# Performance work log

Measured on AMD Instinct MI355X. Metric: run time of the kernel, lower is better.

## Reference

```python
import jax, jax.numpy as jnp
import numpy as np

N = 4096
DIM = 128      # dim_in
HID = 256      # mlp hidden_dim
K_IN = 8       # k for linear_k

def _knn_edges(dist, k):
    # dist: [n,n]; k nearest neighbors excluding self (matches heapq loop)
    n = dist.shape[0]
    d = jnp.where(jnp.eye(n, dtype=bool), jnp.inf, dist)
    nbr = jax.lax.top_k(-d, k)[1]                     # [n,k] indices of k smallest
    src = jnp.repeat(jnp.arange(n), k)                # res[0] = i
    dst = nbr.reshape(-1)                             # res[1] = neighbor
    return src, dst

def _gcn_conv(x, src, dst, W, b):
    # torch_geometric GCNConv: add self loops + symmetric normalization
    n = x.shape[0]
    loop = jnp.arange(n)
    s = jnp.concatenate([src, loop])
    t = jnp.concatenate([dst, loop])
    xw = x @ W
    deg = jax.ops.segment_sum(jnp.ones(s.shape[0], x.dtype), t, num_segments=n)
    dinv = jax.lax.rsqrt(deg)                         # deg >= 1 due to self loops
    norm = dinv[s] * dinv[t]
    out = jax.ops.segment_sum(norm[:, None] * xw[s], t, num_segments=n)
    return out + b

def _gcn(x, src, dst, Wg1, bg1, Wg2, bg2):
    h = jax.nn.relu(_gcn_conv(x, src, dst, Wg1, bg1))
    h = _gcn_conv(h, src, dst, Wg2, bg2)              # dropout is identity in eval
    return jax.nn.log_softmax(h, axis=1)

def _conv2d(x, w, b):
    y = jax.lax.conv_general_dilated(x, w, (1, 1), 'SAME',
        dimension_numbers=('NCHW', 'OIHW', 'NCHW'))
    return y + b.reshape(1, -1, 1, 1)

def setup_inputs():
    key = jax.random.key(0)
    ks = jax.random.split(key, 20)
    f32 = jnp.float32
    def w(k, shape):
        fan = shape[0]
        return (jax.random.uniform(k, shape, f32) * 2 - 1) * (1.0 / np.sqrt(fan))
    return {
        'data_x_1': jax.random.normal(ks[0], (1, N, 4), f32),
        'data_x_2': jax.random.normal(ks[1], (1, N, K_IN, 4), f32),
        'Wk': w(ks[2], (K_IN, 1)),        'bk': jnp.zeros((1,), f32),
        'Wg1': w(ks[3], (8, DIM // 2)),   'bg1': jnp.zeros((DIM // 2,), f32),
        'Wg2': w(ks[4], (DIM // 2, DIM)), 'bg2': jnp.zeros((DIM,), f32),
        'Wq': w(ks[5], (3 * DIM, DIM)),   'bq': jnp.zeros((DIM,), f32),
        'Wkey': w(ks[6], (3 * DIM, DIM)), 'bkey': jnp.zeros((DIM,), f32),
        'Woff': w(ks[7], (4, DIM)),       'boff': jnp.zeros((DIM,), f32),
        'pw': jnp.full((1,), 0.25, f32),
        'Wf1': w(ks[8], (DIM, HID)),      'bf1': jnp.zeros((HID,), f32),
        'Wf2': w(ks[9], (HID, HID)),      'bf2': jnp.zeros((HID,), f32),
        'Wf3': w(ks[10], (HID, 4)),       'bf3': jnp.zeros((4,), f32),
        'Wcy3': w(ks[11], (1, 1, 1, 3)),  'bcy3': jnp.zeros((1,), f32),
        'Wcx3': w(ks[12], (1, 1, 3, 1)),  'bcx3': jnp.zeros((1,), f32),
        'Wcy5': w(ks[13], (1, 1, 1, 5)),  'bcy5': jnp.zeros((1,), f32),
        'Wcx5': w(ks[14], (1, 1, 5, 1)),  'bcx5': jnp.zeros((1,), f32),
        'Wcy9': w(ks[15], (1, 1, 1, 9)),  'bcy9': jnp.zeros((1,), f32),
        'Wcx9': w(ks[16], (1, 1, 9, 1)),  'bcx9': jnp.zeros((1,), f32),
    }

def reference(data_x_1, data_x_2, Wk, bk, Wg1, bg1, Wg2, bg2, Wq, bq, Wkey, bkey,
              Woff, boff, pw, Wf1, bf1, Wf2, bf2, Wf3, bf3,
              Wcy3, bcy3, Wcx3, bcx3, Wcy5, bcy5, Wcx5, bcx5, Wcy9, bcy9, Wcx9, bcx9):
    # linear_k over k dimension: [1,n,k,4] -> transpose -> [1,n,4,k] -> [1,n,4]
    dx2 = jnp.swapaxes(data_x_2, 2, 3)
    dx2_out = (dx2 @ Wk + bk)[..., 0]
    data_x = jnp.concatenate([data_x_1, dx2_out], axis=2)   # [1,n,8]
    Ot = data_x[:, :, 4:]                                   # [1,n,4]

    pos = data_x[:, :, 0:2]
    diff = pos[:, :, None, :] - pos[:, None, :, :]          # [1,n,n,2]
    distances = jnp.linalg.norm(diff, axis=3)               # [1,n,n]
    maxd = jnp.max(distances, axis=2, keepdims=True)
    oushi_atte = 1.0 - distances / maxd                     # [1,n,n]

    x0 = data_x[0]
    dist0 = jax.lax.stop_gradient(distances[0])             # knn on detached dist
    embs = []
    for kk in (3, 5, 9):
        src, dst = _knn_edges(dist0, kk)
        embs.append(_gcn(x0, src, dst, Wg1, bg1, Wg2, bg2)[None])
    embedding = jnp.concatenate(embs, axis=2)               # [1,n,3*DIM]

    query = embedding @ Wq + bq                             # [1,n,DIM]
    key_t = embedding @ Wkey + bkey
    scores = jnp.einsum('bnd,bmd->bnm', query, key_t) / jnp.sqrt(jnp.float32(DIM))
    A = scores / jnp.max(scores, axis=2, keepdims=True)     # [1,n,n]

    A4 = A[None]                                            # [1,1,n,n]
    c3 = _conv2d(A4, Wcy3, bcy3) + _conv2d(A4, Wcx3, bcx3)
    c5 = _conv2d(A4, Wcy5, bcy5) + _conv2d(A4, Wcx5, bcx5)
    c9 = _conv2d(A4, Wcy9, bcy9) + _conv2d(A4, Wcx9, bcx9)

    A_cat = jnp.concatenate([A, oushi_atte, c3[0], c5[0], c9[0]], axis=2)  # [1,n,5n]
    A_cat = (A_cat - A_cat.min()) / (A_cat.max() - A_cat.min())

    Ot5 = jnp.tile(Ot, (1, 5, 1))                           # [1,5n,4]
    h = jnp.matmul(A_cat, Ot5)                              # [1,n,4]
    h = h @ Woff + boff                                     # [1,n,DIM]
    h = jnp.where(h > 0, h, pw * h)                         # PReLU (scalar weight)
    h = jax.nn.relu(h @ Wf1 + bf1)
    h = jax.nn.relu(h @ Wf2 + bf2)
    return h @ Wf3 + bf3                                    # [1,n,4]
```

## Files before the change

kernel.cpp:

```cpp
#include <hip/hip_runtime.h>
#include <math.h>

#define NN 4096

typedef __bf16 bf16x8 __attribute__((ext_vector_type(8)));
typedef float  f32x4  __attribute__((ext_vector_type(4)));

static __device__ __forceinline__ unsigned enc_f(float f){
    unsigned u = __float_as_uint(f);
    return (u & 0x80000000u) ? ~u : (u | 0x80000000u);
}
static __device__ __forceinline__ float dec_f(unsigned u){
    unsigned b = (u & 0x80000000u) ? (u & 0x7fffffffu) : ~u;
    return __uint_as_float(b);
}
static __device__ __forceinline__ float4 shfl4(float4 v, int src){
    float4 r;
    r.x = __shfl(v.x, src, 64);
    r.y = __shfl(v.y, src, 64);
    r.z = __shfl(v.z, src, 64);
    r.w = __shfl(v.w, src, 64);
    return r;
}

__global__ void k_prep(const float* __restrict__ dx1, const float* __restrict__ dx2,
                       const float* __restrict__ Wk, const float* __restrict__ bk,
                       float* __restrict__ x0, float* __restrict__ colsum,
                       float2* __restrict__ pos, float4* __restrict__ otp){
    int n = blockIdx.x*blockDim.x + threadIdx.x;
    if (n >= NN) return;
    float wk[8];
    #pragma unroll
    for (int j=0;j<8;j++) wk[j] = Wk[j];
    float bkv = bk[0];
    float4 d1 = *(const float4*)&dx1[n*4];
    pos[n] = make_float2(d1.x, d1.y);
    #pragma unroll
    for (int c=0;c<4;c++) x0[n*8+c] = (&d1.x)[c];
    float4 ot;
    #pragma unroll
    for (int c=0;c<4;c++){
        float acc = bkv;
        #pragma unroll
        for (int j=0;j<8;j++) acc += dx2[(n*8+j)*4+c]*wk[j];
        x0[n*8+4+c] = acc;
        (&ot.x)[c] = acc;
        atomicAdd(&colsum[c], acc);
    }
    otp[n] = ot;
}

__global__ void k_ty(const float* __restrict__ x0,
        const float* __restrict__ Wcy3, const float* __restrict__ Wcy5, const float* __restrict__ Wcy9,
        float* __restrict__ Ty){
    int j = blockIdx.x*256 + threadIdx.x;
    if (j >= NN) return;
    float Cy[9];
    #pragma unroll
    for (int o=-4;o<=4;o++){
        float c = Wcy9[o+4];
        if (o>=-2 && o<=2) c += Wcy5[o+2];
        if (o>=-1 && o<=1) c += Wcy3[o+1];
        Cy[o+4] = c;
    }
    float4 acc = {0,0,0,0};
    #pragma unroll
    for (int o=-4;o<=4;o++){
        int jj = j - o;
        if ((unsigned)jj < NN){
            float4 ot = *(const float4*)&x0[jj*8+4];
            float c = Cy[o+4];
            acc.x += c*ot.x; acc.y += c*ot.y; acc.z += c*ot.z; acc.w += c*ot.w;
        }
    }
    *(float4*)&Ty[j*4] = acc;
}

__global__ __launch_bounds__(256) void k_dist(const float2* __restrict__ pos,
        const float4* __restrict__ otp,
        float* __restrict__ maxd, int* __restrict__ nbr,
        int* __restrict__ cnt3, int* __restrict__ cnt5, int* __restrict__ cnt9,
        float* __restrict__ dOt){
    int tid = threadIdx.x;
    int lane = tid & 63;
    int i = blockIdx.x*4 + (tid>>6);
    float2 pi = pos[i];
    unsigned long long best[9];
    #pragma unroll
    for (int q=0;q<9;q++) best[q] = ~0ULL;
    float lmax = 0.f;
    float4 dacc = {0,0,0,0};
    for (int t=0;t<64;t++){
        int j = (t<<6) | lane;
        float2 p = pos[j];
        float dx = pi.x - p.x, dy = pi.y - p.y;
        float d = sqrtf(dx*dx + dy*dy);
        lmax = fmaxf(lmax, d);
        float4 otj = otp[j];
        dacc.x += d*otj.x; dacc.y += d*otj.y; dacc.z += d*otj.z; dacc.w += d*otj.w;
        unsigned long long cand = ((unsigned long long)__float_as_uint(d) << 32) | (unsigned)j;
        if (j != i && cand < best[8]){
            best[8] = cand;
            #pragma unroll
            for (int q=8; q>0; --q){
                if (best[q] < best[q-1]){ unsigned long long tm=best[q]; best[q]=best[q-1]; best[q-1]=tm; }
            }
        }
    }
    #pragma unroll
    for (int m=1;m<64;m<<=1){
        lmax = fmaxf(lmax, __shfl_xor(lmax, m, 64));
        dacc.x += __shfl_xor(dacc.x, m, 64);
        dacc.y += __shfl_xor(dacc.y, m, 64);
        dacc.z += __shfl_xor(dacc.z, m, 64);
        dacc.w += __shfl_xor(dacc.w, m, 64);
    }
    if (lane==0){
        maxd[i] = lmax;
        *(float4*)&dOt[i*4] = dacc;
    }
    for (int t=0;t<9;t++){
        unsigned long long w = best[0];
        #pragma unroll
        for (int m=1;m<64;m<<=1){
            unsigned long long o = __shfl_xor(w, m, 64);
            if (o < w) w = o;
        }
        if (best[0] == w){
            #pragma unroll
            for (int q=0;q<8;q++) best[q] = best[q+1];
            best[8] = ~0ULL;
        }
        if (lane==0){
            int j = (int)(w & 0xffffffffu);
            nbr[i*9+t] = j;
            atomicAdd(&cnt9[j], 1);
            if (t<5) atomicAdd(&cnt5[j], 1);
            if (t<3) atomicAdd(&cnt3[j], 1);
        }
    }
}

__global__ __launch_bounds__(256) void k_scan(const int* __restrict__ cnt3,
        const int* __restrict__ cnt5, const int* __restrict__ cnt9,
        int* __restrict__ offc, float* __restrict__ dinvc){
    __shared__ int part[256];
    int tid = threadIdx.x;
    for (int g=0; g<3; g++){
        const int* cp = g==0?cnt3:(g==1?cnt5:cnt9);
        int base = tid*16;
        int loc[16]; int s=0;
        #pragma unroll
        for (int q=0;q<16;q++){ loc[q]=s; s += cp[base+q]; }
        part[tid]=s; __syncthreads();
        for (int d=1; d<256; d<<=1){
            int v = (tid>=d) ? part[tid-d] : 0;
            __syncthreads();
            part[tid] += v;
            __syncthreads();
        }
        int pre = (tid==0) ? 0 : part[tid-1];
        #pragma unroll
        for (int q=0;q<16;q++){
            offc[g*NN + base + q]  = pre + loc[q];
            dinvc[g*NN + base + q] = rsqrtf((float)cp[base+q] + 1.f);
        }
        __syncthreads();
    }
}

__global__ void k_fill(const int* __restrict__ nbr, const int* __restrict__ offc,
        int* __restrict__ cur, int* __restrict__ rev){
    int i = blockIdx.x*256 + threadIdx.x;
    if (i >= NN) return;
    #pragma unroll
    for (int t=0;t<9;t++){
        int j = nbr[i*9+t];
        int gmin = t<3 ? 0 : (t<5 ? 1 : 2);
        for (int g=gmin; g<3; g++){
            int pos = atomicAdd(&cur[g*NN+j], 1);
            int rb = (g==0) ? 0 : (g==1 ? NN*3 : NN*8);
            rev[rb + offc[g*NN+j] + pos] = i;
        }
    }
}

__global__ void k_y1(const float* __restrict__ x0, const float* __restrict__ Wg1,
                     float* __restrict__ xw){
    int idx = blockIdx.x*256 + threadIdx.x;
    if (idx >= NN*64) return;
    int n = idx>>6, c = idx&63;
    float acc = 0.f;
    #pragma unroll
    for (int k=0;k<8;k++) acc += x0[n*8+k]*Wg1[k*64+c];
    xw[idx] = acc;
}

__global__ __launch_bounds__(256) void k_h1y2(const float* __restrict__ xw,
        const int* __restrict__ offc,
        const int* __restrict__ cnt3, const int* __restrict__ cnt5, const int* __restrict__ cnt9,
        const int* __restrict__ rev, const float* __restrict__ dinvc,
        const float* __restrict__ bg1, const float* __restrict__ Wg2,
        float* __restrict__ y2){
    __shared__ float h1s[12][64];
    int n0 = blockIdx.x*4, tid = threadIdx.x;
    for (int s=tid; s<768; s+=256){
        int p = s>>6, k = s&63, g = p>>2, n = n0+(p&3);
        const int* cp = g==0?cnt3:(g==1?cnt5:cnt9);
        int rb = (g==0) ? 0 : (g==1 ? NN*3 : NN*8);
        int cnt = cp[n];
        int o = rb + offc[g*NN+n];
        float dv = dinvc[g*NN+n];
        float srow = dv*xw[n*64+k];
        for (int e=0;e<cnt;e++){
            int i = rev[o+e];
            srow += dinvc[g*NN+i]*xw[i*64+k];
        }
        float v = dv*srow + bg1[k];
        h1s[p][k] = v>0.f ? v : 0.f;
    }
    __syncthreads();
    int c = tid & 127, ph = tid>>7;
    float a6[6] = {0,0,0,0,0,0};
    for (int k=0;k<64;k++){
        float w = Wg2[k*128+c];
        #pragma unroll
        for (int q=0;q<6;q++) a6[q] += h1s[q*2+ph][k]*w;
    }
    #pragma unroll
    for (int q=0;q<6;q++){
        int p = q*2+ph, g = p>>2, n = n0+(p&3);
        float dv = dinvc[g*NN+n];
        y2[(size_t)g*NN*128 + (size_t)n*128 + c] = dv*a6[q];
    }
}

__global__ __launch_bounds__(128) void k_fin(const float* __restrict__ y2,
        const int* __restrict__ offc,
        const int* __restrict__ cnt3, const int* __restrict__ cnt5, const int* __restrict__ cnt9,
        const int* __restrict__ rev, const float* __restrict__ dinvc,
        const float* __restrict__ bg2, float* __restrict__ emb){
    __shared__ float sm[2], ss[2];
    int b = blockIdx.x;
    int n = b & (NN-1), g = b >> 12;
    const int* cp = g==0?cnt3:(g==1?cnt5:cnt9);
    int rb = (g==0) ? 0 : (g==1 ? NN*3 : NN*8);
    int cnt = cp[n];
    int o = rb + offc[g*NN+n];
    float dv = dinvc[g*NN+n];
    int c = threadIdx.x;
    const float* yg = y2 + (size_t)g*NN*128;
    float s = yg[(size_t)n*128 + c];
    for (int e=0;e<cnt;e++){
        int i = rev[o+e];
        s += yg[(size_t)i*128 + c];
    }
    float v = dv*s + bg2[c];
    float m = v;
    #pragma unroll
    for (int st=1;st<64;st<<=1) m = fmaxf(m, __shfl_xor(m, st, 64));
    if ((c&63)==0) sm[c>>6] = m;
    __syncthreads();
    m = fmaxf(sm[0], sm[1]);
    float e = expf(v - m);
    float t = e;
    #pragma unroll
    for (int st=1;st<64;st<<=1) t += __shfl_xor(t, st, 64);
    if ((c&63)==0) ss[c>>6] = t;
    __syncthreads();
    t = ss[0]+ss[1];
    emb[n*384 + g*128 + c] = v - m - logf(t);
}

__global__ __launch_bounds__(256) void k_qk(const float* __restrict__ emb,
        const float* __restrict__ Wq, const float* __restrict__ bq,
        const float* __restrict__ Wkey, const float* __restrict__ bkey,
        __bf16* __restrict__ qh, __bf16* __restrict__ ql,
        __bf16* __restrict__ kh, __bf16* __restrict__ kl){
    __shared__ float es[8][384];
    int n0 = blockIdx.x*8;
    int tid = threadIdx.x;
    for (int idx=tid; idx<8*384; idx+=256){
        int m = idx/384, k = idx%384;
        es[m][k] = emb[(n0+m)*384+k];
    }
    __syncthreads();
    int c = tid & 127;
    int sel = tid >> 7;
    const float* W = sel ? Wkey : Wq;
    float b = sel ? bkey[c] : bq[c];
    float acc[8];
    #pragma unroll
    for (int m=0;m<8;m++) acc[m]=b;
    for (int k=0;k<384;k++){
        float w = W[k*128+c];
        #pragma unroll
        for (int m=0;m<8;m++) acc[m] += es[m][k]*w;
    }
    __bf16* oh = sel ? kh : qh;
    __bf16* ol = sel ? kl : ql;
    #pragma unroll
    for (int m=0;m<8;m++){
        float v = acc[m];
        __bf16 h = (__bf16)v;
        oh[(size_t)(n0+m)*128+c] = h;
        ol[(size_t)(n0+m)*128+c] = (__bf16)(v - (float)h);
    }
}

__global__ __launch_bounds__(256) void k_scores(
        const __bf16* __restrict__ qh, const __bf16* __restrict__ ql,
        const __bf16* __restrict__ kh, const __bf16* __restrict__ kl,
        float* __restrict__ scores,
        unsigned* __restrict__ rowmaxenc, unsigned* __restrict__ rowminenc){
    int bx = blockIdx.x & 31;
    int by = blockIdx.x >> 5;
    int tid = threadIdx.x;
    int w = tid >> 6, lane = tid & 63;
    int li = lane & 15, g = lane >> 4;
    int r0 = by*128 + (w>>1)*64;
    int c0 = bx*128 + (w&1)*64;

    f32x4 acc[4][4] = {};
    for (int ks=0; ks<4; ++ks){
        int kofs = ks*32 + g*8;
        bf16x8 ah[4], al[4], bh[4], bl[4];
        #pragma unroll
        for (int f=0; f<4; ++f){
            ah[f] = *(const bf16x8*)&qh[(size_t)(r0+f*16+li)*128 + kofs];
            al[f] = *(const bf16x8*)&ql[(size_t)(r0+f*16+li)*128 + kofs];
            bh[f] = *(const bf16x8*)&kh[(size_t)(c0+f*16+li)*128 + kofs];
            bl[f] = *(const bf16x8*)&kl[(size_t)(c0+f*16+li)*128 + kofs];
        }
        #pragma unroll
        for (int fr=0; fr<4; ++fr){
            #pragma unroll
            for (int fc=0; fc<4; ++fc){
                acc[fr][fc] = __builtin_amdgcn_mfma_f32_16x16x32_bf16(ah[fr], bh[fc], acc[fr][fc], 0, 0, 0);
                acc[fr][fc] = __builtin_amdgcn_mfma_f32_16x16x32_bf16(ah[fr], bl[fc], acc[fr][fc], 0, 0, 0);
                acc[fr][fc] = __builtin_amdgcn_mfma_f32_16x16x32_bf16(al[fr], bh[fc], acc[fr][fc], 0, 0, 0);
            }
        }
    }
    #pragma unroll
    for (int fr=0; fr<4; ++fr){
        #pragma unroll
        for (int r=0; r<4; ++r){
            int row = r0 + fr*16 + g*4 + r;
            float mx = -INFINITY, mn = INFINITY;
            #pragma unroll
            for (int fc=0; fc<4; ++fc){
                float v = acc[fr][fc][r];
                scores[(size_t)row*NN + c0 + fc*16 + li] = v;
                mx = fmaxf(mx, v);
                mn = fminf(mn, v);
            }
            #pragma unroll
            for (int s=1; s<16; s<<=1){
                mx = fmaxf(mx, __shfl_xor(mx, s, 64));
                mn = fminf(mn, __shfl_xor(mn, s, 64));
            }
            if (li == 0){
                atomicMax(&rowmaxenc[row], enc_f(mx));
                atomicMin(&rowminenc[row], enc_f(mn));
            }
        }
    }
}

__global__ void k_invr(const unsigned* __restrict__ rowmaxenc, float* __restrict__ invr){
    int i = blockIdx.x*256 + threadIdx.x;
    if (i >= NN) return;
    invr[i] = 1.f/dec_f(rowmaxenc[i]);
}

__global__ __launch_bounds__(256) void k_cconv(const float* __restrict__ scores,
        const float* __restrict__ invr,
        const float* __restrict__ Wcy3, const float* __restrict__ Wcx3,
        const float* __restrict__ Wcy5, const float* __restrict__ Wcx5,
        const float* __restrict__ Wcy9, const float* __restrict__ Wcx9,
        const float* __restrict__ bcy3, const float* __restrict__ bcx3,
        const float* __restrict__ bcy5, const float* __restrict__ bcx5,
        const float* __restrict__ bcy9, const float* __restrict__ bcx9,
        float* __restrict__ mnmx){
    __shared__ float smn[4], smx[4];
    int tid = threadIdx.x;
    int w = tid >> 6, lane = tid & 63;
    int strip = blockIdx.x;
    int i0 = (blockIdx.y*4 + w)*19;
    int colbase = strip*248 - 4 + lane*4;
    bool lv = (colbase >= 0) && (colbase + 3 < NN);
    bool outLane = (lane >= 1) && (lane < 63) && lv;

    float wy3[3],wx3[3],wy5[5],wx5[5],wy9[9],wx9[9];
    #pragma unroll
    for (int t=0;t<3;t++){ wy3[t]=Wcy3[t]; wx3[t]=Wcx3[t]; }
    #pragma unroll
    for (int t=0;t<5;t++){ wy5[t]=Wcy5[t]; wx5[t]=Wcx5[t]; }
    #pragma unroll
    for (int t=0;t<9;t++){ wy9[t]=Wcy9[t]; wx9[t]=Wcx9[t]; }
    float bc3 = bcy3[0]+bcx3[0];
    float bc5 = bcy5[0]+bcx5[0];
    float bc9 = bcy9[0]+bcx9[0];

    float4 win[9];
    float mn = INFINITY, mx = -INFINITY;
    const int laneL = lane - 1, laneR = lane + 1;

    for (int tb = 0; tb < 3; ++tb){
        #pragma unroll
        for (int u = 0; u < 9; ++u){
            int t  = tb*9 + u;
            int ri = i0 - 4 + t;
            float4 a = make_float4(0,0,0,0);
            if (((unsigned)ri < NN) && lv){
                float iv = invr[ri];
                float4 v = *(const float4*)&scores[(size_t)ri*NN + colbase];
                a.x = v.x*iv; a.y = v.y*iv; a.z = v.z*iv; a.w = v.w*iv;
            }
            win[u] = a;
            int ro = i0 + t - 8;
            if (t >= 8 && ro < NN){
                float4 ctr = win[(u+5)%9];
                float4 wl = shfl4(ctr, laneL);
                float4 wr = shfl4(ctr, laneR);
                if (outLane){
                    float cw[12] = {wl.x,wl.y,wl.z,wl.w, ctr.x,ctr.y,ctr.z,ctr.w, wr.x,wr.y,wr.z,wr.w};
                    #pragma unroll
                    for (int c=0;c<4;c++){
                        float cx9 = ((win[(u+1)%9][c]*wx9[0] + win[(u+2)%9][c]*wx9[1]) + (win[(u+3)%9][c]*wx9[2] + win[(u+4)%9][c]*wx9[3]))
                                  + ((win[(u+5)%9][c]*wx9[4] + win[(u+6)%9][c]*wx9[5]) + (win[(u+7)%9][c]*wx9[6] + win[(u+8)%9][c]*wx9[7]))
                                  + win[u][c]*wx9[8];
                        float cx5 = ((win[(u+3)%9][c]*wx5[0] + win[(u+4)%9][c]*wx5[1]) + (win[(u+5)%9][c]*wx5[2] + win[(u+6)%9][c]*wx5[3]))
                                  + win[(u+7)%9][c]*wx5[4];
                        float cx3 = (win[(u+4)%9][c]*wx3[0] + win[(u+5)%9][c]*wx3[1]) + win[(u+6)%9][c]*wx3[2];
                        float cy9 = ((cw[c+0]*wy9[0] + cw[c+1]*wy9[1]) + (cw[c+2]*wy9[2] + cw[c+3]*wy9[3]))
                                  + ((cw[c+4]*wy9[4] + cw[c+5]*wy9[5]) + (cw[c+6]*wy9[6] + cw[c+7]*wy9[7]))
                                  + cw[c+8]*wy9[8];
                        float cy5 = ((cw[c+2]*wy5[0] + cw[c+3]*wy5[1]) + (cw[c+4]*wy5[2] + cw[c+5]*wy5[3]))
                                  + cw[c+6]*wy5[4];
                        float cy3 = (cw[c+3]*wy3[0] + cw[c+4]*wy3[1]) + cw[c+5]*wy3[2];
                        float c3v = cy3+cx3+bc3, c5v = cy5+cx5+bc5, c9v = cy9+cx9+bc9;
                        mn = fminf(mn, fminf(fminf(c3v,c5v),c9v));
                        mx = fmaxf(mx, fmaxf(fmaxf(c3v,c5v),c9v));
                    }
                }
            }
        }
    }
    #pragma unroll
    for (int m=1; m<64; m<<=1){
        mn = fminf(mn, __shfl_xor(mn, m, 64));
        mx = fmaxf(mx, __shfl_xor(mx, m, 64));
    }
    if (lane == 0){ smn[w] = mn; smx[w] = mx; }
    __syncthreads();
    if (tid == 0){
        float a0 = fminf(fminf(smn[0],smn[1]), fminf(smn[2],smn[3]));
        float b0 = fmaxf(fmaxf(smx[0],smx[1]), fmaxf(smx[2],smx[3]));
        int bid = blockIdx.y*gridDim.x + blockIdx.x;
        mnmx[bid] = a0;
        mnmx[1024 + bid] = b0;
    }
}

__global__ __launch_bounds__(256) void k_kot(const __bf16* __restrict__ kh, const __bf16* __restrict__ kl,
        const float* __restrict__ x0, const float* __restrict__ Ty,
        float* __restrict__ kOt){
    __shared__ float red[256][8];
    int d = blockIdx.x, tid = threadIdx.x;
    float a[8] = {0,0,0,0,0,0,0,0};
    for (int j = tid; j < NN; j += 256){
        float kv = (float)kh[(size_t)j*128 + d] + (float)kl[(size_t)j*128 + d];
        float4 ot = *(const float4*)&x0[j*8+4];
        float4 ty = *(const float4*)&Ty[j*4];
        a[0] += kv*ot.x; a[1] += kv*ot.y; a[2] += kv*ot.z; a[3] += kv*ot.w;
        a[4] += kv*ty.x; a[5] += kv*ty.y; a[6] += kv*ty.z; a[7] += kv*ty.w;
    }
    #pragma unroll
    for (int q=0;q<8;q++) red[tid][q] = a[q];
    __syncthreads();
    for (int s=128; s>0; s>>=1){
        if (tid < s){
            #pragma unroll
            for (int q=0;q<8;q++) red[tid][q] += red[tid+s][q];
        }
        __syncthreads();
    }
    if (tid < 8) kOt[d*8 + tid] = red[0][tid];
}

__global__ __launch_bounds__(256) void k_asd(
        const __bf16* __restrict__ qh, const __bf16* __restrict__ ql,
        const float* __restrict__ kOt,
        const unsigned* __restrict__ rowmaxenc, const float* __restrict__ maxd,
        const float* __restrict__ dOt, const float* __restrict__ colsum,
        const float* __restrict__ bcy3, const float* __restrict__ bcx3,
        const float* __restrict__ bcy5, const float* __restrict__ bcx5,
        const float* __restrict__ bcy9, const float* __restrict__ bcx9,
        float* __restrict__ ASdot, float* __restrict__ Bv){
    __shared__ float kst[128*8];
    int tid = threadIdx.x;
    for (int s = tid; s < 1024; s += 256) kst[s] = kOt[s];
    __syncthreads();
    int lane = tid & 63, r = tid >> 6;
    int i = blockIdx.x*4 + r;
    float a[8] = {0,0,0,0,0,0,0,0};
    #pragma unroll
    for (int dd=0; dd<2; ++dd){
        int d = lane + dd*64;
        float qv = (float)qh[(size_t)i*128 + d] + (float)ql[(size_t)i*128 + d];
        #pragma unroll
        for (int q=0;q<8;q++) a[q] += qv * kst[d*8+q];
    }
    #pragma unroll
    for (int m=1; m<64; m<<=1){
        #pragma unroll
        for (int q=0;q<8;q++) a[q] += __shfl_xor(a[q], m, 64);
    }
    if (lane == 0){
        float iv = 1.f/dec_f(rowmaxenc[i]);
        float imv = 1.f/maxd[i];
        float bcsum = bcy3[0]+bcx3[0]+bcy5[0]+bcx5[0]+bcy9[0]+bcx9[0];
        float k = 1.f + bcsum;
        float4 cs = *(const float4*)colsum;
        float4 dv = *(const float4*)&dOt[i*4];
        float4 pa = {iv*a[0], iv*a[1], iv*a[2], iv*a[3]};
        float4 b;
        b.x = cs.x*k - imv*dv.x + iv*a[4];
        b.y = cs.y*k - imv*dv.y + iv*a[5];
        b.z = cs.z*k - imv*dv.z + iv*a[6];
        b.w = cs.w*k - imv*dv.w + iv*a[7];
        *(float4*)&ASdot[i*4] = pa;
        *(float4*)&Bv[i*4]    = b;
    }
}

__global__ __launch_bounds__(256) void k_gmm(const float* __restrict__ mnmx,
        const unsigned* __restrict__ rowminenc, const unsigned* __restrict__ rowmaxenc,
        float* __restrict__ gmm){
    __shared__ float smn[256], smx[256];
    int tid = threadIdx.x;
    float mn = 0.f, mx = 1.f;
    for (int i=tid; i<NN; i+=256){
        float rmx = dec_f(rowmaxenc[i]);
        float q = dec_f(rowminenc[i]) / rmx;
        mn = fminf(mn, fminf(1.f, q));
        mx = fmaxf(mx, fmaxf(1.f, q));
    }
    for (int b=tid; b<918; b+=256){
        mn = fminf(mn, mnmx[b]);
        mx = fmaxf(mx, mnmx[1024+b]);
    }
    smn[tid]=mn; smx[tid]=mx; __syncthreads();
    for (int s=128;s>0;s>>=1){
        if (tid<s){ smn[tid]=fminf(smn[tid],smn[tid+s]); smx[tid]=fmaxf(smx[tid],smx[tid+s]); }
        __syncthreads();
    }
    if (tid==0){ gmm[0]=smn[0]; gmm[1]=smx[0]; }
}

__global__ void k_hfin(const float* __restrict__ ASdot, const float* __restrict__ Bv,
        const float* __restrict__ Wcx3, const float* __restrict__ Wcx5, const float* __restrict__ Wcx9,
        const float* __restrict__ gmm, const float* __restrict__ colsum,
        float* __restrict__ hfin){
    int i = blockIdx.x*256 + threadIdx.x;
    if (i >= NN) return;
    float Cx[9];
    #pragma unroll
    for (int o=-4;o<=4;o++){
        float c = Wcx9[o+4];
        if (o>=-2 && o<=2) c += Wcx5[o+2];
        if (o>=-1 && o<=1) c += Wcx3[o+1];
        Cx[o+4] = c;
    }
    float4 h = *(const float4*)&Bv[i*4];
    float4 a0 = *(const float4*)&ASdot[i*4];
    h.x += a0.x; h.y += a0.y; h.z += a0.z; h.w += a0.w;
    #pragma unroll
    for (int o=-4;o<=4;o++){
        int r = i + o;
        if ((unsigned)r < NN){
            float4 av = *(const float4*)&ASdot[r*4];
            float c = Cx[o+4];
            h.x += c*av.x; h.y += c*av.y; h.z += c*av.z; h.w += c*av.w;
        }
    }
    float mnv = gmm[0], mxv = gmm[1];
    float s = 1.f/(mxv-mnv), oa = -mnv*s;
    float4 cs = *(const float4*)colsum;
    float4 out;
    out.x = s*h.x + 5.f*oa*cs.x;
    out.y = s*h.y + 5.f*oa*cs.y;
    out.z = s*h.z + 5.f*oa*cs.z;
    out.w = s*h.w + 5.f*oa*cs.w;
    *(float4*)&hfin[i*4] = out;
}

__global__ __launch_bounds__(256) void k_mlp(const float* __restrict__ hfin,
        const float* __restrict__ Woff, const float* __restrict__ boff, const float* __restrict__ pw,
        const float* __restrict__ Wf1, const float* __restrict__ bf1,
        const float* __restrict__ Wf2, const float* __restrict__ bf2,
        const float* __restrict__ Wf3, const float* __restrict__ bf3,
        float* __restrict__ out){
    __shared__ float h1[8][128];
    __shared__ float h2[8][256];
    __shared__ float h3[8][256];
    int n0 = blockIdx.x*8, tid = threadIdx.x;
    float p = pw[0];
    {
        int c = tid & 127, mb = (tid>>7)*4;
        #pragma unroll
        for (int mm=0; mm<4; mm++){
            int m = mb+mm;
            float v = boff[c];
            #pragma unroll
            for (int k=0;k<4;k++) v += hfin[(n0+m)*4+k]*Woff[k*128+c];
            h1[m][c] = v>0.f ? v : p*v;
        }
    }
    __syncthreads();
    {
        int c = tid;
        float acc[8];
        #pragma unroll
        for (int m=0;m<8;m++) acc[m] = bf1[c];
        for (int k=0;k<128;k++){
            float w = Wf1[k*256+c];
            #pragma unroll
            for (int m=0;m<8;m++) acc[m] += h1[m][k]*w;
        }
        #pragma unroll
        for (int m=0;m<8;m++) h2[m][c] = acc[m]>0.f?acc[m]:0.f;
    }
    __syncthreads();
    {
        int c = tid;
        float acc[8];
        #pragma unroll
        for (int m=0;m<8;m++) acc[m] = bf2[c];
        for (int k=0;k<256;k++){
            float w = Wf2[k*256+c];
            #pragma unroll
            for (int m=0;m<8;m++) acc[m] += h2[m][k]*w;
        }
        #pragma unroll
        for (int m=0;m<8;m++) h3[m][c] = acc[m]>0.f?acc[m]:0.f;
    }
    __syncthreads();
    int w = tid >> 6, lane = tid & 63;
    #pragma unroll
    for (int mm=0; mm<2; ++mm){
        int m = w*2 + mm;
        float4 acc = {0,0,0,0};
        #pragma unroll
        for (int q=0;q<4;q++){
            int k = lane + q*64;
            float hv = h3[m][k];
            float4 w3 = *(const float4*)&Wf3[k*4];
            acc.x += hv*w3.x; acc.y += hv*w3.y; acc.z += hv*w3.z; acc.w += hv*w3.w;
        }
        #pragma unroll
        for (int s=1; s<64; s<<=1){
            acc.x += __shfl_xor(acc.x, s, 64);
            acc.y += __shfl_xor(acc.y, s, 64);
            acc.z += __shfl_xor(acc.z, s, 64);
            acc.w += __shfl_xor(acc.w, s, 64);
        }
        if (lane == 0){
            float4 o;
            o.x = acc.x + bf3[0]; o.y = acc.y + bf3[1];
            o.z = acc.z + bf3[2]; o.w = acc.w + bf3[3];
            *(float4*)&out[(n0+m)*4] = o;
        }
    }
}

extern "C" void kernel_launch(void* const* d_in, const int* in_sizes, int n_in,
                              void* d_out, int out_size, void* d_ws, size_t ws_size,
                              hipStream_t stream){
    const float* dx1  = (const float*)d_in[0];
    const float* dx2  = (const float*)d_in[1];
    const float* Wk   = (const float*)d_in[2];
    const float* bk   = (const float*)d_in[3];
    const float* Wg1  = (const float*)d_in[4];
    const float* bg1  = (const float*)d_in[5];
    const float* Wg2  = (const float*)d_in[6];
    const float* bg2  = (const float*)d_in[7];
    const float* Wq   = (const float*)d_in[8];
    const float* bq   = (const float*)d_in[9];
    const float* Wkey = (const float*)d_in[10];
    const float* bkey = (const float*)d_in[11];
    const float* Woff = (const float*)d_in[12];
    const float* boff = (const float*)d_in[13];
    const float* pw   = (const float*)d_in[14];
    const float* Wf1  = (const float*)d_in[15];
    const float* bf1  = (const float*)d_in[16];
    const float* Wf2  = (const float*)d_in[17];
    const float* bf2  = (const float*)d_in[18];
    const float* Wf3  = (const float*)d_in[19];
    const float* bf3  = (const float*)d_in[20];
    const float* Wcy3 = (const float*)d_in[21];
    const float* bcy3 = (const float*)d_in[22];
    const float* Wcx3 = (const float*)d_in[23];
    const float* bcx3 = (const float*)d_in[24];
    const float* Wcy5 = (const float*)d_in[25];
    const float* bcy5 = (const float*)d_in[26];
    const float* Wcx5 = (const float*)d_in[27];
    const float* bcx5 = (const float*)d_in[28];
    const float* Wcy9 = (const float*)d_in[29];
    const float* bcy9 = (const float*)d_in[30];
    const float* Wcx9 = (const float*)d_in[31];
    const float* bcx9 = (const float*)d_in[32];

    char* ws = (char*)d_ws;
    size_t off = 0;
    auto alloc = [&](size_t b)->void*{ void* p = ws + off; off += (b + 255) & ~(size_t)255; return p; };

    char* zbase = ws + off;
    float*    colsum    = (float*)   alloc(4*4);
    int*      cnt3      = (int*)     alloc((size_t)NN*4);
    int*      cnt5      = (int*)     alloc((size_t)NN*4);
    int*      cnt9      = (int*)     alloc((size_t)NN*4);
    int*      cur       = (int*)     alloc((size_t)3*NN*4);
    unsigned* rowmaxenc = (unsigned*)alloc((size_t)NN*4);
    size_t zbytes = (size_t)((ws + off) - zbase);
    unsigned* rowminenc = (unsigned*)alloc((size_t)NN*4);

    float*  x0    = (float*) alloc((size_t)NN*8*4);
    float2* pos   = (float2*)alloc((size_t)NN*8);
    float4* otp   = (float4*)alloc((size_t)NN*16);
    float*  maxd  = (float*) alloc((size_t)NN*4);
    int*    nbr   = (int*)   alloc((size_t)NN*9*4);
    int*    offc  = (int*)   alloc((size_t)3*NN*4);
    float*  dinvc = (float*) alloc((size_t)3*NN*4);
    int*    rev   = (int*)   alloc((size_t)NN*17*4);
    float*  xw    = (float*) alloc((size_t)NN*64*4);
    float*  y2    = (float*) alloc((size_t)3*NN*128*4);
    float*  emb   = (float*) alloc((size_t)NN*384*4);
    __bf16* qh    = (__bf16*)alloc((size_t)NN*128*2);
    __bf16* ql    = (__bf16*)alloc((size_t)NN*128*2);
    __bf16* kh    = (__bf16*)alloc((size_t)NN*128*2);
    __bf16* kl    = (__bf16*)alloc((size_t)NN*128*2);
    float* scores = (float*)alloc((size_t)NN*NN*4);
    float* Tyb    = (float*)alloc((size_t)NN*4*4);
    float* invr   = (float*)alloc((size_t)NN*4);
    float* dOt    = (float*)alloc((size_t)NN*4*4);
    float* kOt    = (float*)alloc((size_t)128*8*4);
    float* ASd    = (float*)alloc((size_t)NN*4*4);
    float* Bv     = (float*)alloc((size_t)NN*4*4);
    float* mnmx   = (float*)alloc((size_t)2*1024*4);
    float* gmm    = (float*)alloc(2*4);
    float* hfin   = (float*)alloc((size_t)NN*4*4);
    (void)ws_size; (void)in_sizes; (void)n_in; (void)out_size;

    hipMemsetAsync(zbase, 0, zbytes, stream);
    hipMemsetAsync(rowminenc, 0xFF, (size_t)NN*4, stream);

    k_prep<<<16,256,0,stream>>>(dx1,dx2,Wk,bk,x0,colsum,pos,otp);
    k_ty  <<<16,256,0,stream>>>(x0,Wcy3,Wcy5,Wcy9,Tyb);
    k_dist<<<NN/4,256,0,stream>>>(pos,otp,maxd,nbr,cnt3,cnt5,cnt9,dOt);
    k_scan<<<1,256,0,stream>>>(cnt3,cnt5,cnt9,offc,dinvc);
    k_fill<<<16,256,0,stream>>>(nbr,offc,cur,rev);

    k_y1  <<<NN*64/256,256,0,stream>>>(x0,Wg1,xw);
    k_h1y2<<<NN/4,256,0,stream>>>(xw,offc,cnt3,cnt5,cnt9,rev,dinvc,bg1,Wg2,y2);
    k_fin <<<NN*3,128,0,stream>>>(y2,offc,cnt3,cnt5,cnt9,rev,dinvc,bg2,emb);

    k_qk<<<NN/8,256,0,stream>>>(emb,Wq,bq,Wkey,bkey,qh,ql,kh,kl);
    k_scores<<<1024,256,0,stream>>>(qh,ql,kh,kl,scores,rowmaxenc,rowminenc);
    k_invr<<<16,256,0,stream>>>(rowmaxenc,invr);
    k_kot<<<128,256,0,stream>>>(kh,kl,x0,Tyb,kOt);

    k_cconv<<<dim3(17,54),256,0,stream>>>(scores,invr,
        Wcy3,Wcx3,Wcy5,Wcx5,Wcy9,Wcx9,
        bcy3,bcx3,bcy5,bcx5,bcy9,bcx9, mnmx);
    k_asd<<<NN/4,256,0,stream>>>(qh,ql,kOt,rowmaxenc,maxd,dOt,colsum,
        bcy3,bcx3,bcy5,bcx5,bcy9,bcx9, ASd, Bv);
    k_gmm<<<1,256,0,stream>>>(mnmx,rowminenc,rowmaxenc,gmm);
    k_hfin<<<16,256,0,stream>>>(ASd,Bv,Wcx3,Wcx5,Wcx9,gmm,colsum,hfin);
    k_mlp<<<NN/8,256,0,stream>>>(hfin,Woff,boff,pw,Wf1,bf1,Wf2,bf2,Wf3,bf3,(float*)d_out);
}
```

Before: 305.5 us.

## Replace per-lane kNN insertion sort with threshold filter and candidate compaction

The kNN search in k_dist drops each lane's 9-entry register insertion sort. It now tracks only a per-lane minimum distance and takes the 9th smallest of those minima as an upper-bound threshold. A second pass recomputes distances, uses ballot and popcount to compact candidates under the threshold into shared memory (capped at 192), and selects the 9 nearest by wave-wide min reductions. This removes divergent insertion work and lowers register pressure, at the cost of a second distance sweep. Results would be wrong if more than 192 candidates pass the threshold.

```diff
diff --git a/kernel.cpp b/kernel.cpp
--- a/kernel.cpp
+++ b/kernel.cpp
@@ -22,6 +22,11 @@
     r.w = __shfl(v.w, src, 64);
     return r;
 }
+static __device__ __forceinline__ unsigned long long shflx_u64(unsigned long long v, int m){
+    unsigned lo = __shfl_xor((unsigned)(v & 0xffffffffu), m, 64);
+    unsigned hi = __shfl_xor((unsigned)(v >> 32), m, 64);
+    return ((unsigned long long)hi << 32) | lo;
+}
 
 __global__ void k_prep(const float* __restrict__ dx1, const float* __restrict__ dx2,
                        const float* __restrict__ Wk, const float* __restrict__ bk,
@@ -76,19 +81,19 @@
     *(float4*)&Ty[j*4] = acc;
 }
 
+#define KCAP 192
 __global__ __launch_bounds__(256) void k_dist(const float2* __restrict__ pos,
         const float4* __restrict__ otp,
         float* __restrict__ maxd, int* __restrict__ nbr,
         int* __restrict__ cnt3, int* __restrict__ cnt5, int* __restrict__ cnt9,
         float* __restrict__ dOt){
+    __shared__ unsigned long long cbuf[4][KCAP];
     int tid = threadIdx.x;
-    int lane = tid & 63;
-    int i = blockIdx.x*4 + (tid>>6);
+    int w = tid >> 6, lane = tid & 63;
+    int i = blockIdx.x*4 + w;
     float2 pi = pos[i];
-    unsigned long long best[9];
-    #pragma unroll
-    for (int q=0;q<9;q++) best[q] = ~0ULL;
-    float lmax = 0.f;
+
+    float lmax = 0.f, lmin = INFINITY;
     float4 dacc = {0,0,0,0};
     for (int t=0;t<64;t++){
         int j = (t<<6) | lane;
@@ -98,14 +103,7 @@
         lmax = fmaxf(lmax, d);
         float4 otj = otp[j];
         dacc.x += d*otj.x; dacc.y += d*otj.y; dacc.z += d*otj.z; dacc.w += d*otj.w;
-        unsigned long long cand = ((unsigned long long)__float_as_uint(d) << 32) | (unsigned)j;
-        if (j != i && cand < best[8]){
-            best[8] = cand;
-            #pragma unroll
-            for (int q=8; q>0; --q){
-                if (best[q] < best[q-1]){ unsigned long long tm=best[q]; best[q]=best[q-1]; best[q-1]=tm; }
-            }
-        }
+        if (j != i) lmin = fminf(lmin, d);
     }
     #pragma unroll
     for (int m=1;m<64;m<<=1){
@@ -119,24 +117,54 @@
         maxd[i] = lmax;
         *(float4*)&dOt[i*4] = dacc;
     }
-    for (int t=0;t<9;t++){
-        unsigned long long w = best[0];
-        #pragma unroll
-        for (int m=1;m<64;m<<=1){
-            unsigned long long o = __shfl_xor(w, m, 64);
-            if (o < w) w = o;
-        }
-        if (best[0] == w){
-            #pragma unroll
-            for (int q=0;q<8;q++) best[q] = best[q+1];
-            best[8] = ~0ULL;
-        }
-        if (lane==0){
-            int j = (int)(w & 0xffffffffu);
-            nbr[i*9+t] = j;
+    float v = lmin, T = 0.f;
+    #pragma unroll
+    for (int r=0;r<9;r++){
+        float m = v;
+        #pragma unroll
+        for (int s=1;s<64;s<<=1) m = fminf(m, __shfl_xor(m, s, 64));
+        T = m;
+        if (v == m) v = INFINITY;
+    }
+
+    int base = 0;
+    for (int t=0;t<64;t++){
+        int j = (t<<6) | lane;
+        float2 p = pos[j];
+        float dx = pi.x - p.x, dy = pi.y - p.y;
+        float d = sqrtf(dx*dx + dy*dy);
+        bool pass = (j != i) && (d <= T);
+        unsigned long long b = __ballot(pass);
+        if (b){
+            int pre = __popcll(b & ((1ull<<lane)-1ull));
+            int idx = base + pre;
+            if (pass && idx < KCAP)
+                cbuf[w][idx] = ((unsigned long long)__float_as_uint(d) << 32) | (unsigned)j;
+            base += __popcll(b);
+        }
+    }
+    int M = base < KCAP ? base : KCAP;
+
+    unsigned long long c0 = (lane      < M) ? cbuf[w][lane]      : ~0ULL;
+    unsigned long long c1 = (lane+64   < M) ? cbuf[w][lane+64]   : ~0ULL;
+    unsigned long long c2 = (lane+128  < M) ? cbuf[w][lane+128]  : ~0ULL;
+    for (int r=0;r<9;r++){
+        unsigned long long mv = c0 < c1 ? c0 : c1;
+        mv = mv < c2 ? mv : c2;
+        #pragma unroll
+        for (int s=1;s<64;s<<=1){
+            unsigned long long o = shflx_u64(mv, s);
+            if (o < mv) mv = o;
+        }
+        if (c0 == mv) c0 = ~0ULL;
+        else if (c1 == mv) c1 = ~0ULL;
+        else if (c2 == mv) c2 = ~0ULL;
+        if (lane == 0){
+            int j = (int)(mv & 0xffffffffu);
+            nbr[i*9+r] = j;
             atomicAdd(&cnt9[j], 1);
-            if (t<5) atomicAdd(&cnt5[j], 1);
-            if (t<3) atomicAdd(&cnt3[j], 1);
+            if (r<5) atomicAdd(&cnt5[j], 1);
+            if (r<3) atomicAdd(&cnt3[j], 1);
         }
     }
 }
```

Measured after the change: 303.5 us. About the same (-0.7%).
